# Kernel tuning notes

Measured on AMD Instinct MI355X. Metric: run time of the kernel, lower is better.

## Reference

```python
import jax, jax.numpy as jnp
import numpy as np

B, T, D = 2, 2048, 2048
N, K, H = 8, 4, 256
WINDOW = 1024
BASE_FREQ = 10000
ROPE_PROP = 1.0
SCALE_FACTOR = 1.0
K_MASK = -2.3819763e+38


def apply_rope(inputs, positions, base_frequency, scale_factor=1.0, rope_proportion=1.0):
    # inputs: [B,L,N,H], positions: [B,L]
    head_dim = inputs.shape[-1]
    rope_angles = int(rope_proportion * head_dim // 2)
    nope_angles = head_dim // 2 - rope_angles
    freq_exponents = 2.0 / head_dim * jnp.arange(rope_angles, dtype=jnp.float32)
    timescale = jnp.pad(base_frequency ** freq_exponents, (0, nope_angles),
                        mode='constant', constant_values=(0, jnp.inf))
    sinusoid = positions[..., None].astype(jnp.float32) / timescale[None, None, :]
    sinusoid = sinusoid[..., None, :] / scale_factor  # [B,L,1,H//2]
    sin = jnp.sin(sinusoid)
    cos = jnp.cos(sinusoid)
    first, second = jnp.split(inputs, 2, axis=-1)
    out = jnp.concatenate([first * cos - second * sin,
                           second * cos + first * sin], axis=-1)
    return out.astype(inputs.dtype)


def rms_norm(x, scale, eps=1e-6):
    var = jnp.mean(jnp.square(x.astype(jnp.float32)), axis=-1, keepdims=True)
    normed = x * jax.lax.rsqrt(var + eps)
    return (normed * (1.0 + scale)).astype(x.dtype)


def setup_inputs() -> dict:
    key = jax.random.key(0)
    ks = jax.random.split(key, 5)
    std = 0.02
    return {
        'x': jax.random.normal(ks[0], (B, T, D), jnp.float32),
        'positions': jnp.broadcast_to(jnp.arange(T, dtype=jnp.int32), (B, T)),
        'q_w': jax.random.normal(ks[1], (N, D, H), jnp.float32) * std,
        'k_w': jax.random.normal(ks[2], (K, D, H), jnp.float32) * std,
        'v_w': jax.random.normal(ks[3], (K, D, H), jnp.float32) * std,
        'o_w': jax.random.normal(ks[4], (N, H, D), jnp.float32) * std,
        'q_norm_scale': jnp.zeros((H,), jnp.float32),
        'k_norm_scale': jnp.zeros((H,), jnp.float32),
    }


def reference(x, positions, q_w, k_w, v_w, o_w, q_norm_scale, k_norm_scale):
    # QKV projections (Einsum modules)
    q = jnp.einsum('btd,ndh->btnh', x, q_w)   # [B,T,N,H]
    k = jnp.einsum('bsd,kdh->bskh', x, k_w)   # [B,S,K,H]
    v = jnp.einsum('bsd,kdh->bskh', x, v_w)
    # QK RMSNorm (gemma-style, zero-centered scale)
    q = rms_norm(q, q_norm_scale)
    k = rms_norm(k, k_norm_scale)
    # RoPE (local attention: base 10000, full proportion)
    q = apply_rope(q, positions, BASE_FREQ, SCALE_FACTOR, ROPE_PROP)
    k = apply_rope(k, positions, BASE_FREQ, SCALE_FACTOR, ROPE_PROP)
    q = q * (H ** -0.5)
    # GQA: group queries over kv heads
    G = N // K
    qg = q.reshape(B, T, K, G, H)
    logits = jnp.einsum('btkgh,bskh->btkgs', qg, k)  # [B,T,K,G,S]
    # causal + sliding-window mask from positions
    qp = positions[:, :, None]
    kp = positions[:, None, :]
    mask = (kp <= qp) & (kp > qp - WINDOW)           # [B,T,S]
    logits = jnp.where(mask[:, :, None, None, :], logits, K_MASK)
    probs = jax.nn.softmax(logits.astype(jnp.float32), axis=-1).astype(logits.dtype)
    out = jnp.einsum('btkgs,bskh->btkgh', probs, v).reshape(B, T, N, H)
    return jnp.einsum('btnh,nhd->btd', out, o_w)
```

## Files before the change

### kernel.cpp

```cpp
#include <hip/hip_runtime.h>
#include <cmath>

#define T_SEQ 2048
#define WINDOW 1024

typedef __attribute__((ext_vector_type(8))) short bf16x8;
typedef __attribute__((ext_vector_type(4))) float f32x4;
typedef __attribute__((ext_vector_type(16))) float f32x16;

__device__ __forceinline__ unsigned short f2bf(float f) {
  union { float f; unsigned int u; } v; v.f = f;
  unsigned int r = v.u + 0x7FFFu + ((v.u >> 16) & 1u);
  return (unsigned short)(r >> 16);
}
__device__ __forceinline__ float bf2f(unsigned short u) {
  union { unsigned int i; float f; } v; v.i = ((unsigned int)u) << 16;
  return v.f;
}

#define GLD16(gp, lp)                                                  \
  __builtin_amdgcn_global_load_lds(                                    \
      (__attribute__((address_space(1))) unsigned int*)(gp),           \
      (__attribute__((address_space(3))) unsigned int*)(lp), 16, 0, 0)

__global__ __launch_bounds__(256) void prep(
    const float* __restrict__ x,
    const float* __restrict__ qw, const float* __restrict__ kw,
    const float* __restrict__ vw, const float* __restrict__ ow,
    unsigned short* __restrict__ xb, unsigned short* __restrict__ wqkvt,
    unsigned short* __restrict__ wot) {
  __shared__ float tile[64][65];
  const int blk = blockIdx.x;
  const int tid = threadIdx.x;
  if (blk < 8192) {
    size_t i = (size_t)blk * 256 + tid;
    float4 v = *(const float4*)&x[i * 4];
    ushort4 o;
    o.x = f2bf(v.x); o.y = f2bf(v.y); o.z = f2bf(v.z); o.w = f2bf(v.w);
    *(ushort4*)&xb[i * 4] = o;
    return;
  }
  int tx = tid & 15, ty = tid >> 4;
  if (blk < 10240) {
    int idx = blk - 8192;
    int c0 = (idx & 63) * 64, d0 = (idx >> 6) * 64;
    const float* src; int hbase;
    if (c0 < 2048) { src = qw + (size_t)(c0 >> 8) * 524288; hbase = c0 & 255; }
    else if (c0 < 3072) { int cc = c0 - 2048; src = kw + (size_t)(cc >> 8) * 524288; hbase = cc & 255; }
    else { int cc = c0 - 3072; src = vw + (size_t)(cc >> 8) * 524288; hbase = cc & 255; }
#pragma unroll
    for (int p = 0; p < 4; ++p) {
      float4 v = *(const float4*)&src[(size_t)(d0 + ty + 16 * p) * 256 + hbase + tx * 4];
      tile[ty + 16 * p][tx * 4 + 0] = v.x; tile[ty + 16 * p][tx * 4 + 1] = v.y;
      tile[ty + 16 * p][tx * 4 + 2] = v.z; tile[ty + 16 * p][tx * 4 + 3] = v.w;
    }
    __syncthreads();
#pragma unroll
    for (int p = 0; p < 4; ++p) {
      int hh = ty + 16 * p;
      ushort4 o;
      o.x = f2bf(tile[tx * 4 + 0][hh]); o.y = f2bf(tile[tx * 4 + 1][hh]);
      o.z = f2bf(tile[tx * 4 + 2][hh]); o.w = f2bf(tile[tx * 4 + 3][hh]);
      *(ushort4*)&wqkvt[(size_t)(c0 + hh) * 2048 + d0 + tx * 4] = o;
    }
  } else {
    int idx = blk - 10240;
    int j0 = (idx & 31) * 64, d0 = (idx >> 5) * 64;
#pragma unroll
    for (int p = 0; p < 4; ++p) {
      float4 v = *(const float4*)&ow[(size_t)(j0 + ty + 16 * p) * 2048 + d0 + tx * 4];
      tile[ty + 16 * p][tx * 4 + 0] = v.x; tile[ty + 16 * p][tx * 4 + 1] = v.y;
      tile[ty + 16 * p][tx * 4 + 2] = v.z; tile[ty + 16 * p][tx * 4 + 3] = v.w;
    }
    __syncthreads();
#pragma unroll
    for (int p = 0; p < 4; ++p) {
      int hh = ty + 16 * p;
      ushort4 o;
      o.x = f2bf(tile[tx * 4 + 0][hh]); o.y = f2bf(tile[tx * 4 + 1][hh]);
      o.z = f2bf(tile[tx * 4 + 2][hh]); o.w = f2bf(tile[tx * 4 + 3][hh]);
      *(ushort4*)&wot[(size_t)(d0 + hh) * 2048 + j0 + tx * 4] = o;
    }
  }
}

__device__ __forceinline__ void gemm256_core(
    const unsigned short* __restrict__ Ab, const unsigned short* __restrict__ Bb,
    unsigned short* lds, f32x4 acc[8][4], int aoff, int boff) {
  const int tid = threadIdx.x;

  const int l0 = tid, l1 = tid + 512;
  const int r0 = l0 >> 2, o0 = l0 & 3;
  const int r1 = l1 >> 2, o1 = l1 & 3;
  const int sA0 = r0 * 2048 + ((o0 ^ ((r0 >> 2) & 3)) << 3);
  const int sA1 = r1 * 2048 + ((o1 ^ ((r1 >> 2) & 3)) << 3);

#define STAGE(srcbase, kofs, dstbase)                  \
  do {                                                 \
    GLD16((srcbase) + sA0 + (kofs), (dstbase) + l0 * 8); \
    GLD16((srcbase) + sA1 + (kofs), (dstbase) + l1 * 8); \
  } while (0)

  STAGE(Ab, 0,  lds + 0);
  STAGE(Bb, 0,  lds + 16384);
  STAGE(Ab, 32, lds + 8192);
  STAGE(Bb, 32, lds + 24576);
  STAGE(Ab, 64, lds + 32768);
  STAGE(Bb, 64, lds + 49152);
  asm volatile("s_waitcnt vmcnt(8)" ::: "memory");
  __builtin_amdgcn_s_barrier();

  for (int t = 0; t < 32; ++t) {
    const int p = t & 1;
    unsigned short* base = lds + p * 32768;
    unsigned short* xbase = lds + (p ^ 1) * 32768;
    const int t1 = (t < 31) ? t + 1 : 31;
    const int t2 = (t < 30) ? t + 2 : 31;

    bf16x8 a[4], b[4];
#pragma unroll
    for (int i = 0; i < 4; ++i) a[i] = *(const bf16x8*)(base + aoff + i * 512);
#pragma unroll
    for (int j = 0; j < 4; ++j) b[j] = *(const bf16x8*)(base + 16384 + boff + j * 512);
    STAGE(Ab, t1 * 64 + 32, xbase + 8192);
    __builtin_amdgcn_s_barrier();
    asm volatile("s_waitcnt lgkmcnt(0)" ::: "memory");
    __builtin_amdgcn_sched_barrier(0);
    __builtin_amdgcn_s_setprio(1);
#pragma unroll
    for (int i = 0; i < 4; ++i)
#pragma unroll
      for (int j = 0; j < 4; ++j)
        acc[i][j] = __builtin_amdgcn_mfma_f32_16x16x32_bf16(a[i], b[j], acc[i][j], 0, 0, 0);
    __builtin_amdgcn_s_setprio(0);
    __builtin_amdgcn_s_barrier();

#pragma unroll
    for (int i = 0; i < 4; ++i) a[i] = *(const bf16x8*)(base + aoff + (i + 4) * 512);
    STAGE(Bb, t1 * 64 + 32, xbase + 24576);
    __builtin_amdgcn_s_barrier();
    asm volatile("s_waitcnt lgkmcnt(0)" ::: "memory");
    __builtin_amdgcn_sched_barrier(0);
    __builtin_amdgcn_s_setprio(1);
#pragma unroll
    for (int i = 0; i < 4; ++i)
#pragma unroll
      for (int j = 0; j < 4; ++j)
        acc[i + 4][j] = __builtin_amdgcn_mfma_f32_16x16x32_bf16(a[i], b[j], acc[i + 4][j], 0, 0, 0);
    __builtin_amdgcn_s_setprio(0);
    asm volatile("s_waitcnt vmcnt(8)" ::: "memory");
    __builtin_amdgcn_s_barrier();

#pragma unroll
    for (int i = 0; i < 4; ++i) a[i] = *(const bf16x8*)(base + 8192 + aoff + i * 512);
#pragma unroll
    for (int j = 0; j < 4; ++j) b[j] = *(const bf16x8*)(base + 24576 + boff + j * 512);
    STAGE(Ab, t2 * 64, base + 0);
    __builtin_amdgcn_s_barrier();
    asm volatile("s_waitcnt lgkmcnt(0)" ::: "memory");
    __builtin_amdgcn_sched_barrier(0);
    __builtin_amdgcn_s_setprio(1);
#pragma unroll
    for (int i = 0; i < 4; ++i)
#pragma unroll
      for (int j = 0; j < 4; ++j)
        acc[i][j] = __builtin_amdgcn_mfma_f32_16x16x32_bf16(a[i], b[j], acc[i][j], 0, 0, 0);
    __builtin_amdgcn_s_setprio(0);
    __builtin_amdgcn_s_barrier();

#pragma unroll
    for (int i = 0; i < 4; ++i) a[i] = *(const bf16x8*)(base + 8192 + aoff + (i + 4) * 512);
    STAGE(Bb, t2 * 64, base + 16384);
    __builtin_amdgcn_s_barrier();
    asm volatile("s_waitcnt lgkmcnt(0)" ::: "memory");
    __builtin_amdgcn_sched_barrier(0);
    __builtin_amdgcn_s_setprio(1);
#pragma unroll
    for (int i = 0; i < 4; ++i)
#pragma unroll
      for (int j = 0; j < 4; ++j)
        acc[i + 4][j] = __builtin_amdgcn_mfma_f32_16x16x32_bf16(a[i], b[j], acc[i + 4][j], 0, 0, 0);
    __builtin_amdgcn_s_setprio(0);
    asm volatile("s_waitcnt vmcnt(8)" ::: "memory");
    __builtin_amdgcn_s_barrier();
  }
#undef STAGE
}

__global__ __launch_bounds__(512) void gemm_qkv_256(
    const unsigned short* __restrict__ xb, const unsigned short* __restrict__ wt,
    unsigned short* __restrict__ qo, unsigned short* __restrict__ ko,
    unsigned short* __restrict__ vo) {
  __shared__ unsigned short lds[65536];
  const int tid = threadIdx.x;
  const int wave = tid >> 6, lane = tid & 63;
  const int wr = wave >> 2, wc = wave & 3;
  const int fm = lane & 15, fk = lane >> 4;

  const int bid = blockIdx.x;
  const int swz = (bid & 7) * 32 + (bid >> 3);
  const int m0 = (swz >> 4) * 256, n0 = (swz & 15) * 256;

  const int soff = fm * 32 + ((fk ^ ((fm >> 2) & 3)) << 3);
  const int aoff = wr * 4096 + soff;
  const int boff = wc * 2048 + soff;

  f32x4 acc[8][4];
#pragma unroll
  for (int i = 0; i < 8; ++i)
#pragma unroll
    for (int j = 0; j < 4; ++j) acc[i][j] = {0.f, 0.f, 0.f, 0.f};

  gemm256_core(xb + (size_t)m0 * 2048, wt + (size_t)n0 * 2048, lds, acc, aoff, boff);

  unsigned short* obase; int ldo, cb;
  if (n0 < 2048) { obase = qo; ldo = 2048; cb = n0; }
  else if (n0 < 3072) { obase = ko; ldo = 1024; cb = n0 - 2048; }
  else { obase = vo; ldo = 1024; cb = n0 - 3072; }
  const int rbase = m0 + wr * 128 + (lane >> 4) * 4;
  const int cbase = cb + wc * 64 + fm;
#pragma unroll
  for (int i = 0; i < 8; ++i)
#pragma unroll
    for (int j = 0; j < 4; ++j)
#pragma unroll
      for (int r = 0; r < 4; ++r)
        obase[(size_t)(rbase + i * 16 + r) * ldo + cbase + j * 16] = f2bf(acc[i][j][r]);
}

__global__ __launch_bounds__(512) void gemm_out_256(
    const unsigned short* __restrict__ ab, const unsigned short* __restrict__ wot,
    float* __restrict__ out) {
  __shared__ unsigned short lds[65536];
  const int tid = threadIdx.x;
  const int wave = tid >> 6, lane = tid & 63;
  const int wr = wave >> 2, wc = wave & 3;
  const int fm = lane & 15, fk = lane >> 4;

  const int bid = blockIdx.x;
  const int swz = (bid & 7) * 16 + (bid >> 3);
  const int m0 = (swz >> 3) * 256, n0 = (swz & 7) * 256;

  const int soff = fm * 32 + ((fk ^ ((fm >> 2) & 3)) << 3);
  const int aoff = wr * 4096 + soff;
  const int boff = wc * 2048 + soff;

  f32x4 acc[8][4];
#pragma unroll
  for (int i = 0; i < 8; ++i)
#pragma unroll
    for (int j = 0; j < 4; ++j) acc[i][j] = {0.f, 0.f, 0.f, 0.f};

  gemm256_core(ab + (size_t)m0 * 2048, wot + (size_t)n0 * 2048, lds, acc, aoff, boff);

  const int rbase = m0 + wr * 128 + (lane >> 4) * 4;
  const int cbase = n0 + wc * 64 + fm;
#pragma unroll
  for (int i = 0; i < 8; ++i)
#pragma unroll
    for (int j = 0; j < 4; ++j)
#pragma unroll
      for (int r = 0; r < 4; ++r)
        out[(size_t)(rbase + i * 16 + r) * 2048 + cbase + j * 16] = acc[i][j][r];
}

__global__ __launch_bounds__(256) void postproc(
    unsigned short* __restrict__ qb, const unsigned short* __restrict__ kb,
    unsigned short* __restrict__ kpan,
    const unsigned short* __restrict__ vbf, unsigned short* __restrict__ vpan,
    const int* __restrict__ positions,
    const float* __restrict__ qns, const float* __restrict__ kns) {
  const int blk = blockIdx.x;
  const int tid = threadIdx.x;
  if (blk < 12288) {
    int row = blk * 4 + (tid >> 6);
    int lane = tid & 63;
    const unsigned short* src; const float* ns; float extra; int bt;
    bool isq = row < 32768;
    if (isq) {
      src = qb + (size_t)row * 256; ns = qns; extra = 0.0625f; bt = row >> 3;
    } else {
      int r = row - 32768;
      src = kb + (size_t)r * 256; ns = kns; extra = 1.0f; bt = r >> 2;
    }
    int pos = positions[bt];

    ushort4 u = *(const ushort4*)&src[lane << 2];
    float xv[4] = {bf2f(u.x), bf2f(u.y), bf2f(u.z), bf2f(u.w)};
    float ss = xv[0]*xv[0] + xv[1]*xv[1] + xv[2]*xv[2] + xv[3]*xv[3];
#pragma unroll
    for (int off = 1; off < 64; off <<= 1) ss += __shfl_xor(ss, off, 64);
    float rinv = rsqrtf(ss * (1.0f / 256.0f) + 1e-6f);

    float4 sc4 = *(const float4*)&ns[lane << 2];
    xv[0] *= rinv * (1.0f + sc4.x);
    xv[1] *= rinv * (1.0f + sc4.y);
    xv[2] *= rinv * (1.0f + sc4.z);
    xv[3] *= rinv * (1.0f + sc4.w);

    float ov[4];
#pragma unroll
    for (int c = 0; c < 4; ++c) ov[c] = __shfl_xor(xv[c], 32, 64);

    int hr = (lane & 31) << 2;
    float sgn = (lane < 32) ? -1.0f : 1.0f;
    ushort4 w4;
    unsigned short res[4];
#pragma unroll
    for (int c = 0; c < 4; ++c) {
      float invts = exp2f(-(float)(hr + c) * 0.10381025296523007f);
      float angle = (float)pos * invts;
      float sn, cs;
      __sincosf(angle, &sn, &cs);
      res[c] = f2bf((xv[c] * cs + sgn * ov[c] * sn) * extra);
    }
    w4.x = res[0]; w4.y = res[1]; w4.z = res[2]; w4.w = res[3];
    if (isq) {
      *(ushort4*)&qb[(size_t)row * 256 + (lane << 2)] = w4;
    } else {
      int r = row - 32768;
      int kvh = r & 3;
      int b_ = bt >> 11, t = bt & 2047;
      unsigned short* pan = kpan + (((size_t)(b_ * 4 + kvh) * 64 + (t >> 5)) * 8192);
      int s = t & 31;
      int c = lane >> 1;
      size_t el = (size_t)s * 256 + (size_t)((c ^ s) & 31) * 8 + (lane & 1) * 4;
      *(ushort4*)&pan[el] = w4;
    }
    return;
  }
  __shared__ unsigned short tile[64][68];
  int idx = blk - 12288;
  int h0 = (idx & 3) * 64;
  int t0 = ((idx >> 2) & 31) * 64;
  int z = idx >> 7;
  int tx = tid & 15, ty = tid >> 4;
  const unsigned short* src = vbf + ((size_t)(z >> 2) * 8192 + (z & 3)) * 256;
#pragma unroll
  for (int p = 0; p < 4; ++p) {
    ushort4 v = *(const ushort4*)&src[(size_t)(t0 + ty + 16 * p) * 1024 + h0 + tx * 4];
    tile[ty + 16 * p][tx * 4 + 0] = v.x; tile[ty + 16 * p][tx * 4 + 1] = v.y;
    tile[ty + 16 * p][tx * 4 + 2] = v.z; tile[ty + 16 * p][tx * 4 + 3] = v.w;
  }
  __syncthreads();
#pragma unroll
  for (int p = 0; p < 4; ++p) {
    int hh = ty + 16 * p;
    int h = h0 + hh;
    int t = t0 + tx * 4;
    int pp = t >> 5, s = t & 31;
    ushort4 o;
    o.x = tile[tx * 4 + 0][hh]; o.y = tile[tx * 4 + 1][hh];
    o.z = tile[tx * 4 + 2][hh]; o.w = tile[tx * 4 + 3][hh];
    size_t el = ((size_t)z * 64 + pp) * 8192 + (size_t)h * 32 +
                (size_t)(((s >> 3) ^ h ^ (h >> 2)) & 3) * 8 + (s & 7);
    *(ushort4*)&vpan[el] = o;
  }
}

__global__ __launch_bounds__(128) void attn_mfma(
    const unsigned short* __restrict__ qb,
    const unsigned short* __restrict__ kpan,
    const unsigned short* __restrict__ vpan,
    unsigned short* __restrict__ ob) {
  __shared__ __align__(16) unsigned short Kl[8192];
  __shared__ __align__(16) unsigned short Vl[8192];
  __shared__ __align__(16) unsigned short Ps[3072];

  const int tid = threadIdx.x;
  const int w = tid >> 6, lane = tid & 63;
  const int l5 = lane >> 5, l31 = lane & 31;
  const int pair = blockIdx.x & 7;
  const int t0 = (blockIdx.x >> 3) * 32;
  const int kvh = pair >> 1, b = pair & 1;
  const int n = 2 * kvh + w;
  const int tmin = t0, tmax = t0 + 31;

  bf16x8 aq[16];
  {
    const unsigned short* qrow =
        qb + (((size_t)b * 2048 + tmin + l31) * 8 + n) * 256 + l5 * 8;
#pragma unroll
    for (int kc = 0; kc < 16; ++kc) aq[kc] = *(const bf16x8*)(qrow + kc * 16);
  }

  f32x16 O[8], lsum;
#pragma unroll
  for (int i = 0; i < 8; ++i)
#pragma unroll
    for (int r = 0; r < 16; ++r) O[i][r] = 0.f;
#pragma unroll
  for (int r = 0; r < 16; ++r) lsum[r] = 0.f;

  bf16x8 ones;
#pragma unroll
  for (int i = 0; i < 8; ++i) ones[i] = (short)0x3F80;

  const unsigned short* kpb = kpan + (size_t)(b * 4 + kvh) * 64 * 8192;
  const unsigned short* vpb = vpan + (size_t)(b * 4 + kvh) * 64 * 8192;

  int s_lo = t0 - 1024; if (s_lo < 0) s_lo = 0;
  const int s_end = t0 + 32;

  for (int s0 = s_lo; s0 < s_end; s0 += 32) {
    __syncthreads();
    const unsigned short* kp = kpb + (size_t)(s0 >> 5) * 8192;
    const unsigned short* vp = vpb + (size_t)(s0 >> 5) * 8192;
#pragma unroll
    for (int j = 0; j < 8; ++j) {
      int g = j * 128 + tid;
      GLD16(kp + g * 8, Kl + g * 8);
    }
#pragma unroll
    for (int j = 0; j < 8; ++j) {
      int g = j * 128 + tid;
      GLD16(vp + g * 8, Vl + g * 8);
    }
    __syncthreads();

    f32x16 pa, pb;
#pragma unroll
    for (int r = 0; r < 16; ++r) { pa[r] = 0.f; pb[r] = 0.f; }
#pragma unroll
    for (int kc = 0; kc < 16; kc += 2) {
      bf16x8 b0 = *(const bf16x8*)&Kl[l31 * 256 + (((kc * 2 + l5) ^ l31) & 31) * 8];
      bf16x8 b1 = *(const bf16x8*)&Kl[l31 * 256 + ((((kc + 1) * 2 + l5) ^ l31) & 31) * 8];
      pa = __builtin_amdgcn_mfma_f32_32x32x16_bf16(aq[kc], b0, pa, 0, 0, 0);
      pb = __builtin_amdgcn_mfma_f32_32x32x16_bf16(aq[kc + 1], b1, pb, 0, 0, 0);
    }

    bool allvalid = (s0 + 31 <= tmin) && (s0 >= tmax - 1023);
    int scol = s0 + l31;
#pragma unroll
    for (int r = 0; r < 16; ++r) {
      float sv = pa[r] + pb[r];
      float p = exp2f(sv * 1.442695040888963f);
      int m = (r & 3) + 8 * (r >> 2) + 4 * l5;
      if (!allvalid) {
        int dt = (tmin + m) - scol;
        p = (dt >= 0 && dt < 1024) ? p : 0.f;
      }
      Ps[w * 1536 + (l31 >> 4) * 768 + m * 24 + (l31 & 15)] = f2bf(p);
    }

    bf16x8 pf0 = *(const bf16x8*)&Ps[w * 1536 + l31 * 24 + l5 * 8];
    bf16x8 pf1 = *(const bf16x8*)&Ps[w * 1536 + 768 + l31 * 24 + l5 * 8];
    lsum = __builtin_amdgcn_mfma_f32_32x32x16_bf16(pf0, ones, lsum, 0, 0, 0);
    lsum = __builtin_amdgcn_mfma_f32_32x32x16_bf16(pf1, ones, lsum, 0, 0, 0);
#pragma unroll
    for (int hb = 0; hb < 8; ++hb) {
      int row = hb * 32 + l31;
      int gh = (row ^ (row >> 2)) & 3;
      bf16x8 v0 = *(const bf16x8*)&Vl[row * 32 + ((l5 ^ gh) & 3) * 8];
      bf16x8 v1 = *(const bf16x8*)&Vl[row * 32 + (((2 + l5) ^ gh) & 3) * 8];
      O[hb] = __builtin_amdgcn_mfma_f32_32x32x16_bf16(pf0, v0, O[hb], 0, 0, 0);
      O[hb] = __builtin_amdgcn_mfma_f32_32x32x16_bf16(pf1, v1, O[hb], 0, 0, 0);
    }
  }

  unsigned short* obase = ob + (((size_t)b * 2048 + tmin) * 8 + n) * 256;
#pragma unroll
  for (int r = 0; r < 16; ++r) {
    int m = (r & 3) + 8 * (r >> 2) + 4 * l5;
    float rinv = 1.0f / lsum[r];
    size_t rowoff = (size_t)m * 2048;
#pragma unroll
    for (int hb = 0; hb < 8; ++hb)
      obase[rowoff + hb * 32 + l31] = f2bf(O[hb][r] * rinv);
  }
}

extern "C" void kernel_launch(void* const* d_in, const int* in_sizes, int n_in,
                              void* d_out, int out_size, void* d_ws, size_t ws_size,
                              hipStream_t stream) {
  const float* x   = (const float*)d_in[0];
  const int* pos   = (const int*)d_in[1];
  const float* q_w = (const float*)d_in[2];
  const float* k_w = (const float*)d_in[3];
  const float* v_w = (const float*)d_in[4];
  const float* o_w = (const float*)d_in[5];
  const float* qns = (const float*)d_in[6];
  const float* kns = (const float*)d_in[7];
  float* out = (float*)d_out;

  unsigned short* W = (unsigned short*)d_ws;
  unsigned short* qb0   = W;
  unsigned short* kb0   = W + 8388608;
  unsigned short* vbf   = W + 12582912;
  unsigned short* vpan  = W + 16777216;
  unsigned short* kpan  = W + 20971520;
  unsigned short* xb    = W + 25165824;
  unsigned short* wqkvt = W + 33554432;
  unsigned short* abuf  = wqkvt;
  unsigned short* wot   = W + 41943040;

  prep<<<dim3(11264), 256, 0, stream>>>(x, q_w, k_w, v_w, o_w, xb, wqkvt, wot);
  gemm_qkv_256<<<dim3(256), 512, 0, stream>>>(xb, wqkvt, qb0, kb0, vbf);
  postproc<<<dim3(13312), 256, 0, stream>>>(qb0, kb0, kpan, vbf, vpan, pos, qns, kns);
  attn_mfma<<<dim3(512), 128, 0, stream>>>(qb0, kpan, vpan, abuf);
  gemm_out_256<<<dim3(128), 512, 0, stream>>>(abuf, wot, out);
}
```

Before: 346.4 us.

## Halve output GEMM M-tile to 128 rows and reverse attention block order

```diff
diff --git a/kernel.cpp b/kernel.cpp
--- a/kernel.cpp
+++ b/kernel.cpp
@@ -231,32 +231,132 @@
 __global__ __launch_bounds__(512) void gemm_out_256(
     const unsigned short* __restrict__ ab, const unsigned short* __restrict__ wot,
     float* __restrict__ out) {
-  __shared__ unsigned short lds[65536];
+  __shared__ unsigned short lds[49152];
   const int tid = threadIdx.x;
   const int wave = tid >> 6, lane = tid & 63;
   const int wr = wave >> 2, wc = wave & 3;
   const int fm = lane & 15, fk = lane >> 4;
 
   const int bid = blockIdx.x;
-  const int swz = (bid & 7) * 16 + (bid >> 3);
-  const int m0 = (swz >> 3) * 256, n0 = (swz & 7) * 256;
+  const int swz = (bid & 7) * 32 + (bid >> 3);
+  const int m0 = (swz >> 3) * 128, n0 = (swz & 7) * 256;
 
   const int soff = fm * 32 + ((fk ^ ((fm >> 2) & 3)) << 3);
-  const int aoff = wr * 4096 + soff;
+  const int aoff = wr * 2048 + soff;
   const int boff = wc * 2048 + soff;
 
-  f32x4 acc[8][4];
-#pragma unroll
-  for (int i = 0; i < 8; ++i)
+  const unsigned short* Ab = ab + (size_t)m0 * 2048;
+  const unsigned short* Bb = wot + (size_t)n0 * 2048;
+
+  const int ra = tid >> 2, oa = tid & 3;
+  const int sAa = ra * 2048 + ((oa ^ ((ra >> 2) & 3)) << 3);
+  const int id1 = tid + 512;
+  const int rb1 = id1 >> 2, ob1 = id1 & 3;
+  const int sB1 = rb1 * 2048 + ((ob1 ^ ((rb1 >> 2) & 3)) << 3);
+
+#define STAGE_A(kofs, dstbase) GLD16(Ab + sAa + (kofs), (dstbase) + tid * 8)
+#define STAGE_B(kofs, dstbase)                                   \
+  do {                                                           \
+    GLD16(Bb + sAa + (kofs), (dstbase) + tid * 8);               \
+    GLD16(Bb + sB1 + (kofs), (dstbase) + (tid + 512) * 8);       \
+  } while (0)
+
+  f32x4 acc[4][4];
+#pragma unroll
+  for (int i = 0; i < 4; ++i)
 #pragma unroll
     for (int j = 0; j < 4; ++j) acc[i][j] = {0.f, 0.f, 0.f, 0.f};
 
-  gemm256_core(ab + (size_t)m0 * 2048, wot + (size_t)n0 * 2048, lds, acc, aoff, boff);
-
-  const int rbase = m0 + wr * 128 + (lane >> 4) * 4;
+  STAGE_A(0,  lds + 0);
+  STAGE_B(0,  lds + 8192);
+  STAGE_A(32, lds + 4096);
+  STAGE_B(32, lds + 16384);
+  STAGE_A(64, lds + 24576);
+  STAGE_B(64, lds + 24576 + 8192);
+  asm volatile("s_waitcnt vmcnt(6)" ::: "memory");
+  __builtin_amdgcn_s_barrier();
+
+  for (int t = 0; t < 32; ++t) {
+    const int p = t & 1;
+    unsigned short* base = lds + p * 24576;
+    unsigned short* xbase = lds + (p ^ 1) * 24576;
+    const int t1 = (t < 31) ? t + 1 : 31;
+    const int t2 = (t < 30) ? t + 2 : 31;
+
+    bf16x8 a[4], b[2];
+#pragma unroll
+    for (int i = 0; i < 4; ++i) a[i] = *(const bf16x8*)(base + aoff + i * 512);
+#pragma unroll
+    for (int j = 0; j < 2; ++j) b[j] = *(const bf16x8*)(base + 8192 + boff + j * 512);
+    STAGE_A(t1 * 64 + 32, xbase + 4096);
+    __builtin_amdgcn_s_barrier();
+    asm volatile("s_waitcnt lgkmcnt(0)" ::: "memory");
+    __builtin_amdgcn_sched_barrier(0);
+    __builtin_amdgcn_s_setprio(1);
+#pragma unroll
+    for (int i = 0; i < 4; ++i)
+#pragma unroll
+      for (int j = 0; j < 2; ++j)
+        acc[i][j] = __builtin_amdgcn_mfma_f32_16x16x32_bf16(a[i], b[j], acc[i][j], 0, 0, 0);
+    __builtin_amdgcn_s_setprio(0);
+    __builtin_amdgcn_s_barrier();
+
+#pragma unroll
+    for (int j = 0; j < 2; ++j) b[j] = *(const bf16x8*)(base + 8192 + boff + (j + 2) * 512);
+    STAGE_B(t1 * 64 + 32, xbase + 16384);
+    __builtin_amdgcn_s_barrier();
+    asm volatile("s_waitcnt lgkmcnt(0)" ::: "memory");
+    __builtin_amdgcn_sched_barrier(0);
+    __builtin_amdgcn_s_setprio(1);
+#pragma unroll
+    for (int i = 0; i < 4; ++i)
+#pragma unroll
+      for (int j = 0; j < 2; ++j)
+        acc[i][j + 2] = __builtin_amdgcn_mfma_f32_16x16x32_bf16(a[i], b[j], acc[i][j + 2], 0, 0, 0);
+    __builtin_amdgcn_s_setprio(0);
+    asm volatile("s_waitcnt vmcnt(6)" ::: "memory");
+    __builtin_amdgcn_s_barrier();
+
+#pragma unroll
+    for (int i = 0; i < 4; ++i) a[i] = *(const bf16x8*)(base + 4096 + aoff + i * 512);
+#pragma unroll
+    for (int j = 0; j < 2; ++j) b[j] = *(const bf16x8*)(base + 16384 + boff + j * 512);
+    STAGE_A(t2 * 64, base + 0);
+    __builtin_amdgcn_s_barrier();
+    asm volatile("s_waitcnt lgkmcnt(0)" ::: "memory");
+    __builtin_amdgcn_sched_barrier(0);
+    __builtin_amdgcn_s_setprio(1);
+#pragma unroll
+    for (int i = 0; i < 4; ++i)
+#pragma unroll
+      for (int j = 0; j < 2; ++j)
+        acc[i][j] = __builtin_amdgcn_mfma_f32_16x16x32_bf16(a[i], b[j], acc[i][j], 0, 0, 0);
+    __builtin_amdgcn_s_setprio(0);
+    __builtin_amdgcn_s_barrier();
+
+#pragma unroll
+    for (int j = 0; j < 2; ++j) b[j] = *(const bf16x8*)(base + 16384 + boff + (j + 2) * 512);
+    STAGE_B(t2 * 64, base + 8192);
+    __builtin_amdgcn_s_barrier();
+    asm volatile("s_waitcnt lgkmcnt(0)" ::: "memory");
+    __builtin_amdgcn_sched_barrier(0);
+    __builtin_amdgcn_s_setprio(1);
+#pragma unroll
+    for (int i = 0; i < 4; ++i)
+#pragma unroll
+      for (int j = 0; j < 2; ++j)
+        acc[i][j + 2] = __builtin_amdgcn_mfma_f32_16x16x32_bf16(a[i], b[j], acc[i][j + 2], 0, 0, 0);
+    __builtin_amdgcn_s_setprio(0);
+    asm volatile("s_waitcnt vmcnt(6)" ::: "memory");
+    __builtin_amdgcn_s_barrier();
+  }
+#undef STAGE_A
+#undef STAGE_B
+
+  const int rbase = m0 + wr * 64 + (lane >> 4) * 4;
   const int cbase = n0 + wc * 64 + fm;
 #pragma unroll
-  for (int i = 0; i < 8; ++i)
+  for (int i = 0; i < 4; ++i)
 #pragma unroll
     for (int j = 0; j < 4; ++j)
 #pragma unroll
@@ -371,7 +471,7 @@
   const int w = tid >> 6, lane = tid & 63;
   const int l5 = lane >> 5, l31 = lane & 31;
   const int pair = blockIdx.x & 7;
-  const int t0 = (blockIdx.x >> 3) * 32;
+  const int t0 = (63 - (blockIdx.x >> 3)) * 32;
   const int kvh = pair >> 1, b = pair & 1;
   const int n = 2 * kvh + w;
   const int tmin = t0, tmax = t0 + 31;
@@ -498,5 +598,5 @@
   gemm_qkv_256<<<dim3(256), 512, 0, stream>>>(xb, wqkvt, qb0, kb0, vbf);
   postproc<<<dim3(13312), 256, 0, stream>>>(qb0, kb0, kpan, vbf, vpan, pos, qns, kns);
   attn_mfma<<<dim3(512), 128, 0, stream>>>(qb0, kpan, vpan, abuf);
-  gemm_out_256<<<dim3(128), 512, 0, stream>>>(abuf, wot, out);
-}
+  gemm_out_256<<<dim3(256), 512, 0, stream>>>(abuf, wot, out);
+}
```

Result: faster. 335.0 us (-3.3%).
